# Optimization experiments

Hardware: AMD Instinct MI355X
Metric: run time of the kernel (lower is better)

## Reference

```python
import jax, jax.numpy as jnp
import numpy as np

E = 1_600_000      # num edges
N = 50_000         # num nodes
G = 100            # num graphs in batch
EMB = 128          # emb_size
OUT = 256          # out_emb_size
NRAD = 6           # num_radial
NDENSE = 3         # num_dense


def setup_inputs() -> dict:
    key = jax.random.key(0)
    ks = jax.random.split(key, 8)
    m = jax.random.normal(ks[0], (E, EMB), dtype=jnp.float32)
    rbf = jax.random.normal(ks[1], (E, NRAD), dtype=jnp.float32)
    src = jax.random.randint(ks[2], (E,), 0, N, dtype=jnp.int64)
    graph_ids = jnp.sort(jax.random.randint(ks[3], (N,), 0, G, dtype=jnp.int64))
    # parameters (torch Linear convention: W [out, in])
    W_rbf = jax.random.normal(ks[4], (EMB, NRAD), dtype=jnp.float32) / np.sqrt(NRAD)
    W_up = jax.random.normal(ks[5], (OUT, EMB), dtype=jnp.float32) / np.sqrt(EMB)
    W_dense = jax.random.normal(ks[6], (NDENSE, OUT, OUT), dtype=jnp.float32) / np.sqrt(OUT)
    b_dense = jnp.zeros((NDENSE, OUT), dtype=jnp.float32)
    return {"m": m, "rbf": rbf, "src": src, "graph_ids": graph_ids,
            "W_rbf": W_rbf, "W_up": W_up, "W_dense": W_dense, "b_dense": b_dense}


def reference(m, rbf, src, graph_ids, W_rbf, W_up, W_dense, b_dense):
    # edge transform: tmp = m * dense_rbf(rbf)            [E, EMB]
    tmp = m * jnp.einsum('er,fr->ef', rbf, W_rbf)
    # reverse-graph copy_e/sum == scatter-sum onto original src nodes
    t = jax.ops.segment_sum(tmp, src, num_segments=N)     # [N, EMB]
    # up projection (no bias)
    t = jnp.einsum('ne,oe->no', t, W_up)                  # [N, OUT]
    # dense MLP with SiLU
    for i in range(NDENSE):
        t = jax.nn.silu(jnp.einsum('no,po->np', t, W_dense[i]) + b_dense[i])
    # extensive readout: per-graph sum
    out = jax.ops.segment_sum(t, graph_ids, num_segments=G)  # [G, OUT]
    return out
```

## Files before the change

kernel.cpp:

```cpp
#include <hip/hip_runtime.h>
#include <hip/hip_bf16.h>

typedef __attribute__((ext_vector_type(8))) short short8;
typedef __attribute__((ext_vector_type(4))) float f32x4;

#define EMB 128
#define OUT 256
#define NRAD 6
#define NDENSE 3
#define BSH 7
#define MAXBKT 512

static __device__ __forceinline__ unsigned short f32_to_bf16(float f) {
    union { float f; unsigned u; } v; v.f = f;
    unsigned r = v.u + 0x7fffu + ((v.u >> 16) & 1u);
    return (unsigned short)(r >> 16);
}
static __device__ __forceinline__ float bf16_to_f32(unsigned short h) {
    union { unsigned u; float f; } v; v.u = ((unsigned)h) << 16;
    return v.f;
}
static __device__ __forceinline__ float silu(float x) {
    return x / (1.f + __expf(-x));
}
static __device__ __forceinline__ void gload_lds16(const void* gp, void* lp) {
    __builtin_amdgcn_global_load_lds(
        (const __attribute__((address_space(1))) void*)gp,
        (__attribute__((address_space(3))) void*)lp, 16, 0, 0);
}

__global__ __launch_bounds__(256) void init_kernel(
        int* __restrict__ bcnt, const float* __restrict__ Wup,
        const float* __restrict__ Wd, unsigned short* __restrict__ Wbf, int nbkt) {
    int i = blockIdx.x * blockDim.x + threadIdx.x;
    int stride = gridDim.x * blockDim.x;
    for (int j = i; j < nbkt; j += stride) bcnt[j] = 0;
    const int n1 = OUT * EMB, n2 = NDENSE * OUT * OUT;
    for (int j = i; j < n1 + n2; j += stride)
        Wbf[j] = f32_to_bf16(j < n1 ? Wup[j] : Wd[j - n1]);
}

__global__ __launch_bounds__(256) void bhist_kernel(
        const int* __restrict__ src, int* __restrict__ bcnt, int E, int nbkt) {
    __shared__ int h[MAXBKT];
    for (int b = threadIdx.x; b < nbkt; b += 256) h[b] = 0;
    __syncthreads();
    int stride = gridDim.x * blockDim.x;
    for (int e = blockIdx.x * blockDim.x + threadIdx.x; e < E; e += stride)
        atomicAdd(&h[src[e] >> BSH], 1);
    __syncthreads();
    for (int b = threadIdx.x; b < nbkt; b += 256)
        if (h[b]) atomicAdd(&bcnt[b], h[b]);
}

__global__ __launch_bounds__(512) void bscan_kernel(
        const int* __restrict__ bcnt, int* __restrict__ bbase,
        int* __restrict__ gcursor, int nbkt, int E) {
    __shared__ int s[MAXBKT];
    int t = threadIdx.x;
    int v = (t < nbkt) ? bcnt[t] : 0;
    s[t] = v;
    __syncthreads();
    for (int d = 1; d < MAXBKT; d <<= 1) {
        int x = (t >= d) ? s[t - d] : 0;
        __syncthreads();
        s[t] += x;
        __syncthreads();
    }
    if (t < nbkt) {
        int ex = s[t] - v;
        bbase[t] = ex;
        gcursor[t] = ex;
    }
    if (t == 0) bbase[nbkt] = E;
}

__global__ __launch_bounds__(256) void bscatter_kernel(
        const int* __restrict__ src, int* __restrict__ gcursor,
        int2* __restrict__ pairs, int E, int nbkt) {
    __shared__ int h[MAXBKT];
    __shared__ int base[MAXBKT];
    for (int b = threadIdx.x; b < nbkt; b += 256) h[b] = 0;
    __syncthreads();
    const int per = (E + gridDim.x - 1) / gridDim.x;
    const int e0 = blockIdx.x * per;
    const int e1 = min(e0 + per, E);
    for (int e = e0 + threadIdx.x; e < e1; e += 256)
        atomicAdd(&h[src[e] >> BSH], 1);
    __syncthreads();
    for (int b = threadIdx.x; b < nbkt; b += 256)
        base[b] = h[b] ? atomicAdd(&gcursor[b], h[b]) : 0;
    __syncthreads();
    for (int e = e0 + threadIdx.x; e < e1; e += 256) {
        int s = src[e];
        int pos = atomicAdd(&base[s >> BSH], 1);
        pairs[pos] = make_int2(e, s);
    }
}

__global__ __launch_bounds__(256) void local_csr_kernel(
        const int2* __restrict__ pairs, const int* __restrict__ bbase,
        int* __restrict__ offsets, int* __restrict__ perm, int N, int E, int nbkt) {
    __shared__ int cnt[128], exc[128], cur[128];
    const int b = blockIdx.x;
    const int t = threadIdx.x;
    const int n0 = b << BSH;
    const int nn = min(128, N - n0);
    const int p0 = bbase[b], p1 = bbase[b + 1];
    if (t < 128) cnt[t] = 0;
    __syncthreads();
    for (int i = p0 + t; i < p1; i += 256)
        atomicAdd(&cnt[pairs[i].y - n0], 1);
    __syncthreads();
    if (t < 128) exc[t] = cnt[t];
    __syncthreads();
    for (int d = 1; d < 128; d <<= 1) {
        int x = (t >= d && t < 128) ? exc[t - d] : 0;
        __syncthreads();
        if (t < 128) exc[t] += x;
        __syncthreads();
    }
    if (t < 128) {
        int ex = exc[t] - cnt[t];
        cur[t] = ex;
        if (t < nn) offsets[n0 + t] = p0 + ex;
    }
    if (b == 0 && t == 0) offsets[N] = E;
    __syncthreads();
    for (int i = p0 + t; i < p1; i += 256) {
        int2 pr = pairs[i];
        int pos = p0 + atomicAdd(&cur[pr.y - n0], 1);
        perm[pos] = pr.x;
    }
}

__global__ __launch_bounds__(256) void edge_accum_kernel(
        const float* __restrict__ m, const float* __restrict__ rbf,
        const int* __restrict__ perm, const int* __restrict__ offsets,
        const float* __restrict__ W_rbf, uint2* __restrict__ t_pack, int N) {
    const int lane = threadIdx.x & 63;
    const int h = lane >> 5;
    const int c = lane & 31;
    const int gw = blockIdx.x * (blockDim.x >> 6) + (threadIdx.x >> 6);
    const int nwaves = gridDim.x * (blockDim.x >> 6);

    float wk[4][6];
#pragma unroll
    for (int k = 0; k < 4; ++k)
#pragma unroll
        for (int j = 0; j < 6; ++j) wk[k][j] = W_rbf[(4 * c + k) * NRAD + j];

    for (int node = gw; node < N; node += nwaves) {
        const int beg = offsets[node], end = offsets[node + 1];
        float a0 = 0.f, a1 = 0.f, a2 = 0.f, a3 = 0.f;
        int pe = 0;
        if (beg < end) {
            int pi = beg + (lane & 7); if (pi > end - 1) pi = end - 1;
            pe = perm[pi];
        }
        for (int cb = beg; cb < end; cb += 8) {
            int pe_next = 0;
            if (cb + 8 < end) {
                int pi = cb + 8 + (lane & 7); if (pi > end - 1) pi = end - 1;
                pe_next = perm[pi];
            }
#pragma unroll
            for (int p = 0; p < 4; ++p) {
                int e = __shfl(pe, 2 * p + h);
                const float2* rp = (const float2*)(rbf + (size_t)e * NRAD);
                float2 r0 = rp[0], r1 = rp[1], r2 = rp[2];
                float4 mv = *(const float4*)(m + (size_t)e * EMB + 4 * c);
                float g = (cb + 2 * p + h < end) ? 1.f : 0.f;
                float p0 = (wk[0][0]*r0.x + wk[0][1]*r0.y + wk[0][2]*r1.x
                          + wk[0][3]*r1.y + wk[0][4]*r2.x + wk[0][5]*r2.y) * g;
                float p1 = (wk[1][0]*r0.x + wk[1][1]*r0.y + wk[1][2]*r1.x
                          + wk[1][3]*r1.y + wk[1][4]*r2.x + wk[1][5]*r2.y) * g;
                float p2 = (wk[2][0]*r0.x + wk[2][1]*r0.y + wk[2][2]*r1.x
                          + wk[2][3]*r1.y + wk[2][4]*r2.x + wk[2][5]*r2.y) * g;
                float p3 = (wk[3][0]*r0.x + wk[3][1]*r0.y + wk[3][2]*r1.x
                          + wk[3][3]*r1.y + wk[3][4]*r2.x + wk[3][5]*r2.y) * g;
                a0 = fmaf(mv.x, p0, a0);
                a1 = fmaf(mv.y, p1, a1);
                a2 = fmaf(mv.z, p2, a2);
                a3 = fmaf(mv.w, p3, a3);
            }
            pe = pe_next;
        }
        a0 += __shfl_xor(a0, 32);
        a1 += __shfl_xor(a1, 32);
        a2 += __shfl_xor(a2, 32);
        a3 += __shfl_xor(a3, 32);
        if (h == 0) {
            uint2 pk;
            pk.x = (unsigned)f32_to_bf16(a0) | ((unsigned)f32_to_bf16(a1) << 16);
            pk.y = (unsigned)f32_to_bf16(a2) | ((unsigned)f32_to_bf16(a3) << 16);
            t_pack[(size_t)node * 32 + c] = pk;
        }
    }
}

template<int K, int ACT>
__global__ __launch_bounds__(256) void gemm2_kernel(
        const unsigned short* __restrict__ A, const unsigned short* __restrict__ W,
        const float* __restrict__ bias, unsigned short* __restrict__ C, int M) {
    __shared__ char lds[32768];
    char* As = lds;
    char* Ws = lds + 16384;

    const int w    = threadIdx.x >> 6;
    const int lane = threadIdx.x & 63;
    const int r    = lane & 15;
    const int g    = lane >> 4;
    const int wr   = w >> 1;
    const int wc   = w & 1;
    const int row0 = blockIdx.x * 128;
    const int col0 = blockIdx.y * 128;

    f32x4 acc[4][4];
#pragma unroll
    for (int i = 0; i < 4; ++i)
#pragma unroll
        for (int j = 0; j < 4; ++j) acc[i][j] = (f32x4){0.f, 0.f, 0.f, 0.f};

    const int lrow = (lane >> 3);
    const int cdst = (lane & 7) * 16;

    for (int kc = 0; kc < K; kc += 64) {
        if (kc) __syncthreads();
#pragma unroll
        for (int it = 0; it < 4; ++it) {
            int slot = it * 4 + w;
            int row  = slot * 8 + lrow;
            int csrc = cdst ^ ((row & 7) << 4);
            int ga   = row0 + row; if (ga >= M) ga = M - 1;
            gload_lds16((const char*)A + ((size_t)ga * K + kc) * 2 + csrc,
                        As + slot * 1024);
            int gw_  = col0 + row;
            gload_lds16((const char*)W + ((size_t)gw_ * K + kc) * 2 + csrc,
                        Ws + slot * 1024);
        }
        asm volatile("s_waitcnt vmcnt(0)" ::: "memory");
        __syncthreads();

#pragma unroll
        for (int ks = 0; ks < 2; ++ks) {
            short8 af[4], bf[4];
#pragma unroll
            for (int mi = 0; mi < 4; ++mi) {
                int row = wr * 64 + mi * 16 + r;
                int byte = row * 128 + ks * 64 + g * 16;
                byte ^= (r & 7) << 4;
                af[mi] = *(const short8*)(As + byte);
            }
#pragma unroll
            for (int nj = 0; nj < 4; ++nj) {
                int col = wc * 64 + nj * 16 + r;
                int byte = col * 128 + ks * 64 + g * 16;
                byte ^= (r & 7) << 4;
                bf[nj] = *(const short8*)(Ws + byte);
            }
#pragma unroll
            for (int mi = 0; mi < 4; ++mi)
#pragma unroll
                for (int nj = 0; nj < 4; ++nj)
                    acc[mi][nj] = __builtin_amdgcn_mfma_f32_16x16x32_bf16(
                        af[mi], bf[nj], acc[mi][nj], 0, 0, 0);
        }
    }

#pragma unroll
    for (int nj = 0; nj < 4; ++nj) {
        int gcol = col0 + wc * 64 + nj * 16 + r;
        float b = bias ? bias[gcol] : 0.f;
#pragma unroll
        for (int mi = 0; mi < 4; ++mi) {
#pragma unroll
            for (int q = 0; q < 4; ++q) {
                int grow = row0 + wr * 64 + mi * 16 + g * 4 + q;
                if (grow < M) {
                    float x = acc[mi][nj][q] + b;
                    if (ACT) x = silu(x);
                    C[(size_t)grow * OUT + gcol] = f32_to_bf16(x);
                }
            }
        }
    }
}

__global__ __launch_bounds__(256) void graph_partial_kernel(
        const unsigned short* __restrict__ h, const int* __restrict__ gids,
        float* __restrict__ partial, int M) {
    int gph = blockIdx.x, s = blockIdx.y;
    int c = threadIdx.x;
    int lo = 0, hi = M;
    while (lo < hi) { int mid = (lo + hi) >> 1; if (gids[mid] < gph) lo = mid + 1; else hi = mid; }
    int lo2 = lo, hi2 = M;
    while (lo2 < hi2) { int mid = (lo2 + hi2) >> 1; if (gids[mid] < gph + 1) lo2 = mid + 1; else hi2 = mid; }
    int len = lo2 - lo;
    int q = (len + 3) >> 2;
    int b0 = lo + s * q;
    int b1 = b0 + q; if (b1 > lo2) b1 = lo2;
    float a0 = 0.f, a1 = 0.f;
    int n = b0;
    for (; n + 1 < b1; n += 2) {
        a0 += bf16_to_f32(h[(size_t)n * OUT + c]);
        a1 += bf16_to_f32(h[(size_t)(n + 1) * OUT + c]);
    }
    for (; n < b1; ++n) a0 += bf16_to_f32(h[(size_t)n * OUT + c]);
    partial[((size_t)gph * 4 + s) * OUT + c] = a0 + a1;
}

__global__ __launch_bounds__(256) void graph_final_kernel(
        const float* __restrict__ partial, float* __restrict__ out) {
    int gph = blockIdx.x, c = threadIdx.x;
    const float* p = partial + (size_t)gph * 4 * OUT + c;
    out[(size_t)gph * OUT + c] = (p[0] + p[OUT]) + (p[2 * OUT] + p[3 * OUT]);
}

extern "C" void kernel_launch(void* const* d_in, const int* in_sizes, int n_in,
                              void* d_out, int out_size, void* d_ws, size_t ws_size,
                              hipStream_t stream) {
    const float* m         = (const float*)d_in[0];
    const float* rbf       = (const float*)d_in[1];
    const int*   src       = (const int*)d_in[2];
    const int*   gids      = (const int*)d_in[3];
    const float* W_rbf     = (const float*)d_in[4];
    const float* W_up      = (const float*)d_in[5];
    const float* W_dense   = (const float*)d_in[6];
    const float* b_dense   = (const float*)d_in[7];
    float* out = (float*)d_out;

    const int E = in_sizes[2];
    const int N = in_sizes[3];
    const int G = out_size / OUT;
    const int nbkt = (N + 127) >> BSH;

    size_t off = 0;
    auto alloc = [&](size_t bytes) -> void* {
        void* p = (char*)d_ws + off;
        off += (bytes + 255) & ~(size_t)255;
        return p;
    };
    int* bcnt    = (int*)alloc((size_t)MAXBKT * 4);
    int* bbase   = (int*)alloc((size_t)(MAXBKT + 1) * 4);
    int* gcursor = (int*)alloc((size_t)MAXBKT * 4);
    int* offsets = (int*)alloc(((size_t)N + 1) * 4);
    int2* pairs  = (int2*)alloc((size_t)E * 8);
    int* perm    = (int*)alloc((size_t)E * 4);
    unsigned short* t_bf = (unsigned short*)alloc((size_t)N * EMB * 2);
    unsigned short* h0   = (unsigned short*)alloc((size_t)N * OUT * 2);
    unsigned short* h1   = (unsigned short*)alloc((size_t)N * OUT * 2);
    float* partial       = (float*)alloc((size_t)G * 4 * OUT * 4);
    unsigned short* Wbf  = (unsigned short*)alloc((size_t)(OUT * EMB + NDENSE * OUT * OUT) * 2);
    unsigned short* Wup_bf = Wbf;
    unsigned short* Wd_bf  = Wbf + OUT * EMB;

    init_kernel<<<512, 256, 0, stream>>>(bcnt, W_up, W_dense, Wbf, nbkt);

    bhist_kernel<<<256, 256, 0, stream>>>(src, bcnt, E, nbkt);
    bscan_kernel<<<1, MAXBKT, 0, stream>>>(bcnt, bbase, gcursor, nbkt, E);
    bscatter_kernel<<<512, 256, 0, stream>>>(src, gcursor, pairs, E, nbkt);
    local_csr_kernel<<<nbkt, 256, 0, stream>>>(pairs, bbase, offsets, perm, N, E, nbkt);

    edge_accum_kernel<<<2048, 256, 0, stream>>>(m, rbf, perm, offsets, W_rbf,
                                                (uint2*)t_bf, N);

    dim3 ggrid((N + 127) / 128, 2);
    gemm2_kernel<EMB, 0><<<ggrid, 256, 0, stream>>>(t_bf, Wup_bf, nullptr, h0, N);
    gemm2_kernel<OUT, 1><<<ggrid, 256, 0, stream>>>(h0, Wd_bf + 0 * OUT * OUT, b_dense + 0 * OUT, h1, N);
    gemm2_kernel<OUT, 1><<<ggrid, 256, 0, stream>>>(h1, Wd_bf + 1 * OUT * OUT, b_dense + 1 * OUT, h0, N);
    gemm2_kernel<OUT, 1><<<ggrid, 256, 0, stream>>>(h0, Wd_bf + 2 * OUT * OUT, b_dense + 2 * OUT, h1, N);

    graph_partial_kernel<<<dim3(G, 4), 256, 0, stream>>>(h1, gids, partial, N);
    graph_final_kernel<<<G, 256, 0, stream>>>(partial, out);
}
```

Baseline: 477.5 us.

## Drop global atomics in histogram, widen edge prefetch, fuse graph readout via atomics

The bucket histogram now writes per-block partial counts that the scan kernel reduces, so the global atomics and the counter zeroing go away. The init kernel zeroes the output instead. The edge accumulation loop processes 16 edges per chunk instead of 8, giving more loads in flight per iteration. The final graph reduction kernel is removed: partial sums are atomically added into the zeroed output, saving one launch but making the float summation order nondeterministic.

```diff
diff --git a/kernel.cpp b/kernel.cpp
--- a/kernel.cpp
+++ b/kernel.cpp
@@ -10,6 +10,7 @@
 #define NDENSE 3
 #define BSH 7
 #define MAXBKT 512
+#define HB 256
 
 static __device__ __forceinline__ unsigned short f32_to_bf16(float f) {
     union { float f; unsigned u; } v; v.f = f;
@@ -30,18 +31,18 @@
 }
 
 __global__ __launch_bounds__(256) void init_kernel(
-        int* __restrict__ bcnt, const float* __restrict__ Wup,
-        const float* __restrict__ Wd, unsigned short* __restrict__ Wbf, int nbkt) {
+        const float* __restrict__ Wup, const float* __restrict__ Wd,
+        unsigned short* __restrict__ Wbf, float* __restrict__ out, int outn) {
     int i = blockIdx.x * blockDim.x + threadIdx.x;
     int stride = gridDim.x * blockDim.x;
-    for (int j = i; j < nbkt; j += stride) bcnt[j] = 0;
+    for (int j = i; j < outn; j += stride) out[j] = 0.f;
     const int n1 = OUT * EMB, n2 = NDENSE * OUT * OUT;
     for (int j = i; j < n1 + n2; j += stride)
         Wbf[j] = f32_to_bf16(j < n1 ? Wup[j] : Wd[j - n1]);
 }
 
 __global__ __launch_bounds__(256) void bhist_kernel(
-        const int* __restrict__ src, int* __restrict__ bcnt, int E, int nbkt) {
+        const int* __restrict__ src, int* __restrict__ bpart, int E, int nbkt) {
     __shared__ int h[MAXBKT];
     for (int b = threadIdx.x; b < nbkt; b += 256) h[b] = 0;
     __syncthreads();
@@ -49,16 +50,18 @@
     for (int e = blockIdx.x * blockDim.x + threadIdx.x; e < E; e += stride)
         atomicAdd(&h[src[e] >> BSH], 1);
     __syncthreads();
-    for (int b = threadIdx.x; b < nbkt; b += 256)
-        if (h[b]) atomicAdd(&bcnt[b], h[b]);
+    int* row = bpart + (size_t)blockIdx.x * MAXBKT;
+    for (int b = threadIdx.x; b < nbkt; b += 256) row[b] = h[b];
 }
 
 __global__ __launch_bounds__(512) void bscan_kernel(
-        const int* __restrict__ bcnt, int* __restrict__ bbase,
+        const int* __restrict__ bpart, int* __restrict__ bbase,
         int* __restrict__ gcursor, int nbkt, int E) {
     __shared__ int s[MAXBKT];
     int t = threadIdx.x;
-    int v = (t < nbkt) ? bcnt[t] : 0;
+    int v = 0;
+    if (t < nbkt)
+        for (int k = 0; k < HB; ++k) v += bpart[(size_t)k * MAXBKT + t];
     s[t] = v;
     __syncthreads();
     for (int d = 1; d < MAXBKT; d <<= 1) {
@@ -155,17 +158,17 @@
         float a0 = 0.f, a1 = 0.f, a2 = 0.f, a3 = 0.f;
         int pe = 0;
         if (beg < end) {
-            int pi = beg + (lane & 7); if (pi > end - 1) pi = end - 1;
+            int pi = beg + (lane & 15); if (pi > end - 1) pi = end - 1;
             pe = perm[pi];
         }
-        for (int cb = beg; cb < end; cb += 8) {
+        for (int cb = beg; cb < end; cb += 16) {
             int pe_next = 0;
-            if (cb + 8 < end) {
-                int pi = cb + 8 + (lane & 7); if (pi > end - 1) pi = end - 1;
+            if (cb + 16 < end) {
+                int pi = cb + 16 + (lane & 15); if (pi > end - 1) pi = end - 1;
                 pe_next = perm[pi];
             }
 #pragma unroll
-            for (int p = 0; p < 4; ++p) {
+            for (int p = 0; p < 8; ++p) {
                 int e = __shfl(pe, 2 * p + h);
                 const float2* rp = (const float2*)(rbf + (size_t)e * NRAD);
                 float2 r0 = rp[0], r1 = rp[1], r2 = rp[2];
@@ -289,7 +292,7 @@
 
 __global__ __launch_bounds__(256) void graph_partial_kernel(
         const unsigned short* __restrict__ h, const int* __restrict__ gids,
-        float* __restrict__ partial, int M) {
+        float* __restrict__ out, int M) {
     int gph = blockIdx.x, s = blockIdx.y;
     int c = threadIdx.x;
     int lo = 0, hi = M;
@@ -307,14 +310,8 @@
         a1 += bf16_to_f32(h[(size_t)(n + 1) * OUT + c]);
     }
     for (; n < b1; ++n) a0 += bf16_to_f32(h[(size_t)n * OUT + c]);
-    partial[((size_t)gph * 4 + s) * OUT + c] = a0 + a1;
-}
-
-__global__ __launch_bounds__(256) void graph_final_kernel(
-        const float* __restrict__ partial, float* __restrict__ out) {
-    int gph = blockIdx.x, c = threadIdx.x;
-    const float* p = partial + (size_t)gph * 4 * OUT + c;
-    out[(size_t)gph * OUT + c] = (p[0] + p[OUT]) + (p[2 * OUT] + p[3 * OUT]);
+    float v = a0 + a1;
+    if (b0 < b1) atomicAdd(&out[(size_t)gph * OUT + c], v);
 }
 
 extern "C" void kernel_launch(void* const* d_in, const int* in_sizes, int n_in,
@@ -341,7 +338,7 @@
         off += (bytes + 255) & ~(size_t)255;
         return p;
     };
-    int* bcnt    = (int*)alloc((size_t)MAXBKT * 4);
+    int* bpart   = (int*)alloc((size_t)HB * MAXBKT * 4);
     int* bbase   = (int*)alloc((size_t)(MAXBKT + 1) * 4);
     int* gcursor = (int*)alloc((size_t)MAXBKT * 4);
     int* offsets = (int*)alloc(((size_t)N + 1) * 4);
@@ -350,15 +347,13 @@
     unsigned short* t_bf = (unsigned short*)alloc((size_t)N * EMB * 2);
     unsigned short* h0   = (unsigned short*)alloc((size_t)N * OUT * 2);
     unsigned short* h1   = (unsigned short*)alloc((size_t)N * OUT * 2);
-    float* partial       = (float*)alloc((size_t)G * 4 * OUT * 4);
     unsigned short* Wbf  = (unsigned short*)alloc((size_t)(OUT * EMB + NDENSE * OUT * OUT) * 2);
     unsigned short* Wup_bf = Wbf;
     unsigned short* Wd_bf  = Wbf + OUT * EMB;
 
-    init_kernel<<<512, 256, 0, stream>>>(bcnt, W_up, W_dense, Wbf, nbkt);
-
-    bhist_kernel<<<256, 256, 0, stream>>>(src, bcnt, E, nbkt);
-    bscan_kernel<<<1, MAXBKT, 0, stream>>>(bcnt, bbase, gcursor, nbkt, E);
+    bhist_kernel<<<HB, 256, 0, stream>>>(src, bpart, E, nbkt);
+    init_kernel<<<512, 256, 0, stream>>>(W_up, W_dense, Wbf, out, out_size);
+    bscan_kernel<<<1, MAXBKT, 0, stream>>>(bpart, bbase, gcursor, nbkt, E);
     bscatter_kernel<<<512, 256, 0, stream>>>(src, gcursor, pairs, E, nbkt);
     local_csr_kernel<<<nbkt, 256, 0, stream>>>(pairs, bbase, offsets, perm, N, E, nbkt);
 
@@ -371,6 +366,5 @@
     gemm2_kernel<OUT, 1><<<ggrid, 256, 0, stream>>>(h1, Wd_bf + 1 * OUT * OUT, b_dense + 1 * OUT, h0, N);
     gemm2_kernel<OUT, 1><<<ggrid, 256, 0, stream>>>(h0, Wd_bf + 2 * OUT * OUT, b_dense + 2 * OUT, h1, N);
 
-    graph_partial_kernel<<<dim3(G, 4), 256, 0, stream>>>(h1, gids, partial, N);
-    graph_final_kernel<<<G, 256, 0, stream>>>(partial, out);
-}
+    graph_partial_kernel<<<dim3(G, 4), 256, 0, stream>>>(h1, gids, out, N);
+}
```

Measured after the change: 450.8 us. -5.6%, faster.
